# Kernel tuning notes

Hardware: AMD Instinct MI355X
Metric: run time of the kernel (lower is better)

The kernel has to match this reference:

```python
import jax, jax.numpy as jnp
import numpy as np

B = 4096          # number of sessions
MEAN_LEN = 50     # mean items per session
N = B * MEAN_LEN  # total items (ragged lengths sum to this)
H = 256           # feat_input_dim == context_input_dim == hidden_dim


def setup_inputs() -> dict:
    key = jax.random.key(0)
    k1, k2, k3, k4, k5, k6, k7 = jax.random.split(key, 7)
    # ragged lengths in [20, 80] adjusted so they sum exactly to N
    rng = np.random.default_rng(0)
    lens = rng.integers(20, 81, size=B)
    lens = (lens * (N / lens.sum())).astype(np.int64)
    lens[-1] += N - lens.sum()
    s = 1.0 / np.sqrt(H)
    return {
        "feats": jax.random.normal(k1, (N, H), jnp.float32),
        "feat_context": jax.random.normal(k2, (N, H), jnp.float32),
        "batch_num_items": jnp.asarray(lens, jnp.int64),
        "Wu": jax.random.uniform(k3, (H, H), jnp.float32, -s, s),
        "bu": jax.random.uniform(k4, (H,), jnp.float32, -s, s),
        "Wv": jax.random.uniform(k5, (H, H), jnp.float32, -s, s),
        "We": jax.random.uniform(k6, (H,), jnp.float32, -s, s),
        "Wout": jax.random.uniform(k7, (H, H), jnp.float32, -s, s),
    }


def reference(feats, feat_context, batch_num_items, Wu, bu, Wv, We, Wout):
    n = feats.shape[0]
    b = batch_num_items.shape[0]
    # additive attention score per item
    feat_u = feats @ Wu.T + bu                     # [N, H]
    feat_v = feat_context @ Wv.T                   # [N, H]
    e = jax.nn.sigmoid(feat_u + feat_v) @ We       # [N]
    # segment ids from ragged lengths (static total length => jit-safe)
    seg = jnp.repeat(jnp.arange(b), batch_num_items, total_repeat_length=n)
    # segment softmax (numerically stable)
    m = jax.ops.segment_max(e, seg, num_segments=b)        # [B]
    ex = jnp.exp(e - m[seg])                               # [N]
    denom = jax.ops.segment_sum(ex, seg, num_segments=b)   # [B]
    alpha = ex / denom[seg]                                # [N]
    # weighted segment-sum pooling
    rst = jax.ops.segment_sum(feats * alpha[:, None], seg, num_segments=b)  # [B, H]
    return rst @ Wout.T
```

## Files before the change

### kernel.cpp

```cpp
#include <hip/hip_runtime.h>
#include <hip/hip_bf16.h>
#include <cstdint>
#include <cstddef>

#define H 256
#define CHUNK 128

typedef __attribute__((ext_vector_type(8))) short    frag8;
typedef __attribute__((ext_vector_type(4))) float    f32x4;
typedef __attribute__((ext_vector_type(4))) uint32_t u32x4;
typedef __attribute__((ext_vector_type(8))) unsigned short ushort8;

__device__ __forceinline__ unsigned short f32_to_bf16(float f) {
    uint32_t u = __float_as_uint(f);
    u = (u + 0x7FFFu + ((u >> 16) & 1u)) >> 16;
    return (unsigned short)u;
}

__device__ __forceinline__ uint32_t pk_bf16(float a, float b) {
    union { __hip_bfloat162 h2; uint32_t u; } cv;
    cv.h2 = __float22bfloat162_rn(make_float2(a, b));
    return cv.u;
}

__global__ void prep(const float* __restrict__ Wu, const float* __restrict__ Wv,
                     const float* __restrict__ Wout,
                     unsigned short* __restrict__ Wopt, float* __restrict__ WoutT) {
    int bid = blockIdx.x, tid = threadIdx.x;
    if (bid < 64) {
        int idx  = bid * 256 + tid;
        int lane = idx & 63;
        int ct   = (idx >> 6) & 15;
        int ksg  = idx >> 10;
        int col  = ct * 16 + (lane & 15);
        int kg   = ksg * 32 + (lane >> 4) * 8;
        ushort8 pk;
        #pragma unroll
        for (int j = 0; j < 8; j++) {
            int k = kg + j;
            float v = (k < 256) ? Wu[col * 256 + k] : Wv[col * 256 + (k - 256)];
            pk[j] = f32_to_bf16(v);
        }
        *(ushort8*)&Wopt[(size_t)idx * 8] = pk;
    } else {
        int t2 = (bid - 64) * 256 + tid;
        int j = t2 & 255, k = t2 >> 8;
        WoutT[t2] = Wout[j * 256 + k];
    }
}

__global__ void seg_offsets(const int* __restrict__ lens, int B, int* __restrict__ off,
                            int2* __restrict__ chunks, int* __restrict__ chunk_cnt) {
    __shared__ int partL[256], partC[256];
    int tid = threadIdx.x;
    bool is64 = (B >= 3) && (lens[1] == 0) && (lens[3] == 0) && (lens[5] == 0);
    int per = (B + 255) / 256;
    int base = tid * per;
    int sL = 0, sC = 0;
    for (int i = 0; i < per; i++) {
        int idx = base + i;
        if (idx < B) {
            int l = is64 ? lens[2 * idx] : lens[idx];
            sL += l;
            sC += (l + CHUNK - 1) / CHUNK;
        }
    }
    partL[tid] = sL; partC[tid] = sC;
    __syncthreads();
    for (int d = 1; d < 256; d <<= 1) {
        int vL = partL[tid], vC = partC[tid];
        int aL = (tid >= d) ? partL[tid - d] : 0;
        int aC = (tid >= d) ? partC[tid - d] : 0;
        __syncthreads();
        partL[tid] = vL + aL; partC[tid] = vC + aC;
        __syncthreads();
    }
    int runL = partL[tid] - sL;
    int runC = partC[tid] - sC;
    for (int i = 0; i < per; i++) {
        int idx = base + i;
        if (idx < B) {
            int l = is64 ? lens[2 * idx] : lens[idx];
            off[idx] = runL;
            int n = (l + CHUNK - 1) / CHUNK;
            for (int c = 0; c < n; c++)
                chunks[runC + c] = make_int2(idx, runL + c * CHUNK);
            runC += n;
            runL += l;
        }
    }
    if (tid == 255) { off[B] = partL[255]; chunk_cnt[0] = partC[255]; }
}

__global__ __launch_bounds__(512, 4) void fused_e(
        const float* __restrict__ feats, const float* __restrict__ ctx,
        const unsigned short* __restrict__ Wopt,
        const float* __restrict__ bu, const float* __restrict__ We,
        float* __restrict__ e_out, int nTiles) {
    __shared__ unsigned short a_lds[2][64 * 128];
    __shared__ float e_part[8 * 64];

    const int tid  = threadIdx.x;
    const int lane = tid & 63;
    const int w    = tid >> 6;
    const int l15  = lane & 15;
    const int q    = lane >> 4;
    const int r0   = tid >> 3;
    const int c8   = tid & 7;
    const int swz  = r0 & 15;
    const int G    = gridDim.x;

    if (blockIdx.x >= nTiles) return;

    float buv[2], wev[2];
    #pragma unroll
    for (int ci = 0; ci < 2; ++ci) {
        int col = w * 32 + ci * 16 + l15;
        buv[ci] = bu[col];
        wev[ci] = We[col];
    }

    f32x4 acc[4][2];
    #pragma unroll
    for (int i = 0; i < 4; i++)
        #pragma unroll
        for (int j = 0; j < 2; j++)
            acc[i][j] = (f32x4)(0.0f);

    f32x4 pre[4];
    auto loadA = [&](int tile, int kt) {
        const float* s = (kt < 2) ? feats : ctx;
        const float* p = s + ((size_t)tile * 64 + r0) * H + ((kt & 1) << 7) + (c8 << 4);
        pre[0] = *(const f32x4*)p;       pre[1] = *(const f32x4*)(p + 4);
        pre[2] = *(const f32x4*)(p + 8); pre[3] = *(const f32x4*)(p + 12);
    };
    auto cvt_store = [&](int buf) {
        u32x4 g0, g1;
        g0[0] = pk_bf16(pre[0][0], pre[0][1]); g0[1] = pk_bf16(pre[0][2], pre[0][3]);
        g0[2] = pk_bf16(pre[1][0], pre[1][1]); g0[3] = pk_bf16(pre[1][2], pre[1][3]);
        g1[0] = pk_bf16(pre[2][0], pre[2][1]); g1[1] = pk_bf16(pre[2][2], pre[2][3]);
        g1[2] = pk_bf16(pre[3][0], pre[3][1]); g1[3] = pk_bf16(pre[3][2], pre[3][3]);
        *(u32x4*)&a_lds[buf][r0 * 128 + (((2 * c8    ) ^ swz) * 8)] = g0;
        *(u32x4*)&a_lds[buf][r0 * 128 + (((2 * c8 + 1) ^ swz) * 8)] = g1;
    };

    loadA(blockIdx.x, 0);
    cvt_store(0);
    loadA(blockIdx.x, 1);
    __syncthreads();

    int cur = 0;
    for (int tile = blockIdx.x; tile < nTiles; tile += G) {
        #pragma unroll
        for (int kt = 0; kt < 4; ++kt) {
            frag8 bfr[4][2];
            #pragma unroll
            for (int ks = 0; ks < 4; ++ks)
                #pragma unroll
                for (int ci = 0; ci < 2; ++ci)
                    bfr[ks][ci] = *(const frag8*)&Wopt[
                        (((size_t)(kt * 4 + ks) * 16 + (w * 2 + ci)) * 64 + lane) * 8];

            #pragma unroll
            for (int ks = 0; ks < 4; ++ks) {
                frag8 afr[4];
                #pragma unroll
                for (int rt = 0; rt < 4; ++rt)
                    afr[rt] = *(const frag8*)&a_lds[cur][(rt * 16 + l15) * 128 + (((ks * 4 + q) ^ l15) * 8)];
                #pragma unroll
                for (int rt = 0; rt < 4; ++rt)
                    #pragma unroll
                    for (int ci = 0; ci < 2; ++ci)
                        acc[rt][ci] = __builtin_amdgcn_mfma_f32_16x16x32_bf16(
                            afr[rt], bfr[ks][ci], acc[rt][ci], 0, 0, 0);
            }

            const bool last_step = (kt == 3) && (tile + G >= nTiles);
            if (!last_step) {
                cvt_store(cur ^ 1);
                int kt2 = kt + 2, tile2 = tile;
                if (kt2 >= 4) { kt2 -= 4; tile2 += G; }
                if (tile2 < nTiles) loadA(tile2, kt2);
            }
            cur ^= 1;
            __syncthreads();
        }

        #pragma unroll
        for (int rt = 0; rt < 4; ++rt) {
            #pragma unroll
            for (int r = 0; r < 4; ++r) {
                float s = 0.0f;
                #pragma unroll
                for (int ci = 0; ci < 2; ++ci) {
                    float h = acc[rt][ci][r] + buv[ci];
                    s += wev[ci] * __builtin_amdgcn_rcpf(1.0f + __expf(-h));
                    acc[rt][ci][r] = 0.0f;
                }
                s += __shfl_xor(s, 1, 64);
                s += __shfl_xor(s, 2, 64);
                s += __shfl_xor(s, 4, 64);
                s += __shfl_xor(s, 8, 64);
                if (l15 == 0) e_part[w * 64 + rt * 16 + q * 4 + r] = s;
            }
        }
        __syncthreads();
        if (tid < 64) {
            float s = 0.0f;
            #pragma unroll
            for (int ww = 0; ww < 8; ++ww) s += e_part[ww * 64 + tid];
            e_out[(size_t)tile * 64 + tid] = s;
        }
        __syncthreads();
    }
}

__global__ __launch_bounds__(256) void seg_stats(
        float* __restrict__ e, const int* __restrict__ off, int B) {
    int seg = blockIdx.x * 4 + (threadIdx.x >> 6);
    int lane = threadIdx.x & 63;
    if (seg >= B) return;
    int start = off[seg];
    int len = off[seg + 1] - start;
    if (len <= CHUNK) return;
    float m = -3.0e38f;
    for (int i = lane; i < len; i += 64) m = fmaxf(m, e[start + i]);
    #pragma unroll
    for (int o = 32; o > 0; o >>= 1) m = fmaxf(m, __shfl_xor(m, o, 64));
    float s = 0.0f;
    for (int i = lane; i < len; i += 64) s += __expf(e[start + i] - m);
    #pragma unroll
    for (int o = 32; o > 0; o >>= 1) s += __shfl_xor(s, o, 64);
    float inv = (s > 0.0f) ? 1.0f / s : 0.0f;
    for (int i = lane; i < len; i += 64) e[start + i] = __expf(e[start + i] - m) * inv;
}

__global__ __launch_bounds__(256) void pool_chunks(
        const float* __restrict__ ealpha, const float* __restrict__ feats,
        const int* __restrict__ off, const int2* __restrict__ chunks,
        const int* __restrict__ chunk_cnt, float* __restrict__ rst) {
    __shared__ float redf[4 * 256];
    __shared__ float smred[8];
    int idx = blockIdx.x;
    if (idx >= chunk_cnt[0]) return;
    int2 en = chunks[idx];
    int seg = en.x, cstart = en.y;
    int sstart = off[seg], send = off[seg + 1];
    int clen = send - cstart;
    if (clen > CHUNK) clen = CHUNK;
    int tid = threadIdx.x, lane = tid & 63, g = tid >> 6;
    const bool multi = (send - sstart) > CHUNK;

    float m = 0.0f, inv = 1.0f;
    if (!multi) {
        float v = (tid < clen) ? ealpha[cstart + tid] : -3.0e38f;
        #pragma unroll
        for (int o = 32; o > 0; o >>= 1) v = fmaxf(v, __shfl_xor(v, o, 64));
        if (lane == 0) smred[g] = v;
        __syncthreads();
        m = fmaxf(fmaxf(smred[0], smred[1]), fmaxf(smred[2], smred[3]));
        float x = (tid < clen) ? __expf(ealpha[cstart + tid] - m) : 0.0f;
        #pragma unroll
        for (int o = 32; o > 0; o >>= 1) x += __shfl_xor(x, o, 64);
        if (lane == 0) smred[4 + g] = x;
        __syncthreads();
        float ssum = smred[4] + smred[5] + smred[6] + smred[7];
        inv = (ssum > 0.0f) ? 1.0f / ssum : 0.0f;
    }

    const f32x4* F = (const f32x4*)feats + (size_t)cstart * 64 + lane;
    const float* A = ealpha + cstart;
    f32x4 acc0 = (f32x4)(0.0f), acc1 = (f32x4)(0.0f);
    int i = g;
    for (; i + 4 < clen; i += 8) {
        float w0 = A[i], w1 = A[i + 4];
        if (!multi) { w0 = __expf(w0 - m) * inv; w1 = __expf(w1 - m) * inv; }
        acc0 += w0 * F[(size_t)i * 64];
        acc1 += w1 * F[(size_t)(i + 4) * 64];
    }
    if (i < clen) {
        float w0 = A[i];
        if (!multi) w0 = __expf(w0 - m) * inv;
        acc0 += w0 * F[(size_t)i * 64];
    }
    acc0 += acc1;
    *(f32x4*)&redf[g * 256 + lane * 4] = acc0;
    __syncthreads();
    float v = redf[tid] + redf[256 + tid] + redf[512 + tid] + redf[768 + tid];
    if (multi) atomicAdd(&rst[(size_t)seg * H + tid], v);
    else rst[(size_t)seg * H + tid] = v;
}

#define RB 8
__global__ __launch_bounds__(256) void out_gemm(
        const float* __restrict__ rst, const float* __restrict__ WoutT,
        float* __restrict__ out) {
    __shared__ float r[RB * 256];
    const int tid = threadIdx.x;
    const size_t b0 = (size_t)blockIdx.x * RB;
    for (int i = tid; i < RB * 256; i += 256) r[i] = rst[b0 * 256 + i];
    __syncthreads();
    float acc[RB];
    #pragma unroll
    for (int j = 0; j < RB; j++) acc[j] = 0.0f;
    for (int k = 0; k < 256; k += 4) {
        f32x4 rw[RB];
        #pragma unroll
        for (int j = 0; j < RB; j++) rw[j] = *(const f32x4*)&r[j * 256 + k];
        #pragma unroll
        for (int kk = 0; kk < 4; kk++) {
            float wv = WoutT[(size_t)(k + kk) * 256 + tid];
            #pragma unroll
            for (int j = 0; j < RB; j++) acc[j] += rw[j][kk] * wv;
        }
    }
    #pragma unroll
    for (int j = 0; j < RB; j++) out[(b0 + j) * 256 + tid] = acc[j];
}

extern "C" void kernel_launch(void* const* d_in, const int* in_sizes, int n_in,
                              void* d_out, int out_size, void* d_ws, size_t ws_size,
                              hipStream_t stream) {
    const float* feats = (const float*)d_in[0];
    const float* ctx   = (const float*)d_in[1];
    const int*   lens  = (const int*)d_in[2];
    const float* Wu    = (const float*)d_in[3];
    const float* bu    = (const float*)d_in[4];
    const float* Wv    = (const float*)d_in[5];
    const float* We    = (const float*)d_in[6];
    const float* Wout  = (const float*)d_in[7];
    float* out = (float*)d_out;

    const int N = in_sizes[0] / H;
    const int B = in_sizes[2];
    const int maxChunks = B + (N + CHUNK - 1) / CHUNK;
    const int nTiles = N / 64;

    char* w = (char*)d_ws;
    auto carve = [&](size_t bytes) {
        char* p = w;
        w += (bytes + 255) & ~(size_t)255;
        return p;
    };
    int*            off    = (int*)           carve((size_t)(B + 1) * sizeof(int));
    float*          e      = (float*)         carve((size_t)N * sizeof(float));
    float*          rst    = (float*)         carve((size_t)B * H * sizeof(float));
    unsigned short* Wopt   = (unsigned short*)carve((size_t)16 * 16 * 64 * 8 * sizeof(unsigned short));
    float*          WoutT  = (float*)         carve((size_t)H * H * sizeof(float));
    int2*           chunks = (int2*)          carve((size_t)maxChunks * sizeof(int2));
    int*            ccnt   = (int*)           carve(sizeof(int));

    hipMemsetAsync(rst, 0, (size_t)B * H * sizeof(float), stream);

    const int gE = (nTiles < 512) ? nTiles : 512;

    prep        <<<320,         256, 0, stream>>>(Wu, Wv, Wout, Wopt, WoutT);
    seg_offsets <<<1,           256, 0, stream>>>(lens, B, off, chunks, ccnt);
    fused_e     <<<gE,          512, 0, stream>>>(feats, ctx, Wopt, bu, We, e, nTiles);
    seg_stats   <<<(B + 3) / 4, 256, 0, stream>>>(e, off, B);
    pool_chunks <<<maxChunks,   256, 0, stream>>>(e, feats, off, chunks, ccnt, rst);
    out_gemm    <<<B / RB,      256, 0, stream>>>(rst, WoutT, out);
}
```

Measured before the change: 583.7 us.

## Merge prep and scan kernels; launch one block per tile in fused_e

The single-block segment-offset scan is folded into the weight-prep kernel as one extra block, which removes a kernel launch and lets the scan run alongside the weight repacking. fused_e drops its persistent grid-stride loop over tiles and launches one block per 64-row tile (N/64 blocks). Inside each block the four K steps are unrolled, with two register prefetch sets keeping loads ahead of the LDS stores. This removes cross-tile loop overhead and raises parallelism, at the cost of more block launches, reloading the B fragments in every block, and no reuse across tiles.

```diff
diff --git a/kernel.cpp b/kernel.cpp
--- a/kernel.cpp
+++ b/kernel.cpp
@@ -23,9 +23,12 @@
     return cv.u;
 }
 
-__global__ void prep(const float* __restrict__ Wu, const float* __restrict__ Wv,
-                     const float* __restrict__ Wout,
-                     unsigned short* __restrict__ Wopt, float* __restrict__ WoutT) {
+__global__ void prep_scan(const float* __restrict__ Wu, const float* __restrict__ Wv,
+                          const float* __restrict__ Wout,
+                          unsigned short* __restrict__ Wopt, float* __restrict__ WoutT,
+                          const int* __restrict__ lens, int B, int* __restrict__ off,
+                          int2* __restrict__ chunks, int* __restrict__ chunk_cnt) {
+    __shared__ int partL[256], partC[256];
     int bid = blockIdx.x, tid = threadIdx.x;
     if (bid < 64) {
         int idx  = bid * 256 + tid;
@@ -42,61 +45,56 @@
             pk[j] = f32_to_bf16(v);
         }
         *(ushort8*)&Wopt[(size_t)idx * 8] = pk;
-    } else {
+    } else if (bid < 320) {
         int t2 = (bid - 64) * 256 + tid;
         int j = t2 & 255, k = t2 >> 8;
         WoutT[t2] = Wout[j * 256 + k];
-    }
-}
-
-__global__ void seg_offsets(const int* __restrict__ lens, int B, int* __restrict__ off,
-                            int2* __restrict__ chunks, int* __restrict__ chunk_cnt) {
-    __shared__ int partL[256], partC[256];
-    int tid = threadIdx.x;
-    bool is64 = (B >= 3) && (lens[1] == 0) && (lens[3] == 0) && (lens[5] == 0);
-    int per = (B + 255) / 256;
-    int base = tid * per;
-    int sL = 0, sC = 0;
-    for (int i = 0; i < per; i++) {
-        int idx = base + i;
-        if (idx < B) {
-            int l = is64 ? lens[2 * idx] : lens[idx];
-            sL += l;
-            sC += (l + CHUNK - 1) / CHUNK;
-        }
-    }
-    partL[tid] = sL; partC[tid] = sC;
-    __syncthreads();
-    for (int d = 1; d < 256; d <<= 1) {
-        int vL = partL[tid], vC = partC[tid];
-        int aL = (tid >= d) ? partL[tid - d] : 0;
-        int aC = (tid >= d) ? partC[tid - d] : 0;
+    } else {
+        bool is64 = (B >= 3) && (lens[1] == 0) && (lens[3] == 0) && (lens[5] == 0);
+        int per = (B + 255) / 256;
+        int base = tid * per;
+        int sL = 0, sC = 0;
+        for (int i = 0; i < per; i++) {
+            int idx = base + i;
+            if (idx < B) {
+                int l = is64 ? lens[2 * idx] : lens[idx];
+                sL += l;
+                sC += (l + CHUNK - 1) / CHUNK;
+            }
+        }
+        partL[tid] = sL; partC[tid] = sC;
         __syncthreads();
-        partL[tid] = vL + aL; partC[tid] = vC + aC;
-        __syncthreads();
-    }
-    int runL = partL[tid] - sL;
-    int runC = partC[tid] - sC;
-    for (int i = 0; i < per; i++) {
-        int idx = base + i;
-        if (idx < B) {
-            int l = is64 ? lens[2 * idx] : lens[idx];
-            off[idx] = runL;
-            int n = (l + CHUNK - 1) / CHUNK;
-            for (int c = 0; c < n; c++)
-                chunks[runC + c] = make_int2(idx, runL + c * CHUNK);
-            runC += n;
-            runL += l;
-        }
-    }
-    if (tid == 255) { off[B] = partL[255]; chunk_cnt[0] = partC[255]; }
+        for (int d = 1; d < 256; d <<= 1) {
+            int vL = partL[tid], vC = partC[tid];
+            int aL = (tid >= d) ? partL[tid - d] : 0;
+            int aC = (tid >= d) ? partC[tid - d] : 0;
+            __syncthreads();
+            partL[tid] = vL + aL; partC[tid] = vC + aC;
+            __syncthreads();
+        }
+        int runL = partL[tid] - sL;
+        int runC = partC[tid] - sC;
+        for (int i = 0; i < per; i++) {
+            int idx = base + i;
+            if (idx < B) {
+                int l = is64 ? lens[2 * idx] : lens[idx];
+                off[idx] = runL;
+                int n = (l + CHUNK - 1) / CHUNK;
+                for (int c = 0; c < n; c++)
+                    chunks[runC + c] = make_int2(idx, runL + c * CHUNK);
+                runC += n;
+                runL += l;
+            }
+        }
+        if (tid == 255) { off[B] = partL[255]; chunk_cnt[0] = partC[255]; }
+    }
 }
 
 __global__ __launch_bounds__(512, 4) void fused_e(
         const float* __restrict__ feats, const float* __restrict__ ctx,
         const unsigned short* __restrict__ Wopt,
         const float* __restrict__ bu, const float* __restrict__ We,
-        float* __restrict__ e_out, int nTiles) {
+        float* __restrict__ e_out) {
     __shared__ unsigned short a_lds[2][64 * 128];
     __shared__ float e_part[8 * 64];
 
@@ -105,12 +103,10 @@
     const int w    = tid >> 6;
     const int l15  = lane & 15;
     const int q    = lane >> 4;
+    const size_t m0 = (size_t)blockIdx.x * 64;
     const int r0   = tid >> 3;
     const int c8   = tid & 7;
     const int swz  = r0 & 15;
-    const int G    = gridDim.x;
-
-    if (blockIdx.x >= nTiles) return;
 
     float buv[2], wev[2];
     #pragma unroll
@@ -127,92 +123,90 @@
         for (int j = 0; j < 2; j++)
             acc[i][j] = (f32x4)(0.0f);
 
-    f32x4 pre[4];
-    auto loadA = [&](int tile, int kt) {
-        const float* s = (kt < 2) ? feats : ctx;
-        const float* p = s + ((size_t)tile * 64 + r0) * H + ((kt & 1) << 7) + (c8 << 4);
-        pre[0] = *(const f32x4*)p;       pre[1] = *(const f32x4*)(p + 4);
-        pre[2] = *(const f32x4*)(p + 8); pre[3] = *(const f32x4*)(p + 12);
-    };
-    auto cvt_store = [&](int buf) {
-        u32x4 g0, g1;
-        g0[0] = pk_bf16(pre[0][0], pre[0][1]); g0[1] = pk_bf16(pre[0][2], pre[0][3]);
-        g0[2] = pk_bf16(pre[1][0], pre[1][1]); g0[3] = pk_bf16(pre[1][2], pre[1][3]);
-        g1[0] = pk_bf16(pre[2][0], pre[2][1]); g1[1] = pk_bf16(pre[2][2], pre[2][3]);
-        g1[2] = pk_bf16(pre[3][0], pre[3][1]); g1[3] = pk_bf16(pre[3][2], pre[3][3]);
-        *(u32x4*)&a_lds[buf][r0 * 128 + (((2 * c8    ) ^ swz) * 8)] = g0;
-        *(u32x4*)&a_lds[buf][r0 * 128 + (((2 * c8 + 1) ^ swz) * 8)] = g1;
-    };
-
-    loadA(blockIdx.x, 0);
-    cvt_store(0);
-    loadA(blockIdx.x, 1);
-    __syncthreads();
-
-    int cur = 0;
-    for (int tile = blockIdx.x; tile < nTiles; tile += G) {
-        #pragma unroll
-        for (int kt = 0; kt < 4; ++kt) {
-            frag8 bfr[4][2];
-            #pragma unroll
-            for (int ks = 0; ks < 4; ++ks)
-                #pragma unroll
-                for (int ci = 0; ci < 2; ++ci)
-                    bfr[ks][ci] = *(const frag8*)&Wopt[
-                        (((size_t)(kt * 4 + ks) * 16 + (w * 2 + ci)) * 64 + lane) * 8];
-
-            #pragma unroll
-            for (int ks = 0; ks < 4; ++ks) {
-                frag8 afr[4];
-                #pragma unroll
-                for (int rt = 0; rt < 4; ++rt)
-                    afr[rt] = *(const frag8*)&a_lds[cur][(rt * 16 + l15) * 128 + (((ks * 4 + q) ^ l15) * 8)];
-                #pragma unroll
-                for (int rt = 0; rt < 4; ++rt)
-                    #pragma unroll
-                    for (int ci = 0; ci < 2; ++ci)
-                        acc[rt][ci] = __builtin_amdgcn_mfma_f32_16x16x32_bf16(
-                            afr[rt], bfr[ks][ci], acc[rt][ci], 0, 0, 0);
-            }
-
-            const bool last_step = (kt == 3) && (tile + G >= nTiles);
-            if (!last_step) {
-                cvt_store(cur ^ 1);
-                int kt2 = kt + 2, tile2 = tile;
-                if (kt2 >= 4) { kt2 -= 4; tile2 += G; }
-                if (tile2 < nTiles) loadA(tile2, kt2);
-            }
-            cur ^= 1;
-            __syncthreads();
-        }
-
-        #pragma unroll
-        for (int rt = 0; rt < 4; ++rt) {
-            #pragma unroll
-            for (int r = 0; r < 4; ++r) {
-                float s = 0.0f;
-                #pragma unroll
-                for (int ci = 0; ci < 2; ++ci) {
-                    float h = acc[rt][ci][r] + buv[ci];
-                    s += wev[ci] * __builtin_amdgcn_rcpf(1.0f + __expf(-h));
-                    acc[rt][ci][r] = 0.0f;
-                }
-                s += __shfl_xor(s, 1, 64);
-                s += __shfl_xor(s, 2, 64);
-                s += __shfl_xor(s, 4, 64);
-                s += __shfl_xor(s, 8, 64);
-                if (l15 == 0) e_part[w * 64 + rt * 16 + q * 4 + r] = s;
-            }
-        }
-        __syncthreads();
-        if (tid < 64) {
+    f32x4 pa0, pa1, pa2, pa3, pb0, pb1, pb2, pb3;
+
+#define LOADA(d0, d1, d2, d3, kt_) do {                                          \
+    const float* _s = ((kt_) < 2) ? feats : ctx;                                 \
+    const float* _p = _s + (m0 + r0) * H + (((kt_) & 1) << 7) + (c8 << 4);       \
+    d0 = *(const f32x4*)_p;       d1 = *(const f32x4*)(_p + 4);                  \
+    d2 = *(const f32x4*)(_p + 8); d3 = *(const f32x4*)(_p + 12); } while (0)
+
+#define CVTST(buf_, s0, s1, s2, s3) do {                                         \
+    u32x4 g0, g1;                                                                \
+    g0[0] = pk_bf16(s0[0], s0[1]); g0[1] = pk_bf16(s0[2], s0[3]);                \
+    g0[2] = pk_bf16(s1[0], s1[1]); g0[3] = pk_bf16(s1[2], s1[3]);                \
+    g1[0] = pk_bf16(s2[0], s2[1]); g1[1] = pk_bf16(s2[2], s2[3]);                \
+    g1[2] = pk_bf16(s3[0], s3[1]); g1[3] = pk_bf16(s3[2], s3[3]);                \
+    *(u32x4*)&a_lds[buf_][r0 * 128 + (((2 * c8    ) ^ swz) * 8)] = g0;           \
+    *(u32x4*)&a_lds[buf_][r0 * 128 + (((2 * c8 + 1) ^ swz) * 8)] = g1; } while (0)
+
+#define STEP(kt_, buf_) do {                                                     \
+    _Pragma("unroll")                                                            \
+    for (int ks = 0; ks < 4; ++ks) {                                             \
+        frag8 bfr[2];                                                            \
+        _Pragma("unroll")                                                        \
+        for (int ci = 0; ci < 2; ++ci)                                           \
+            bfr[ci] = *(const frag8*)&Wopt[                                      \
+                (((size_t)((kt_) * 4 + ks) * 16 + (w * 2 + ci)) * 64 + lane) * 8]; \
+        frag8 afr[4];                                                            \
+        _Pragma("unroll")                                                        \
+        for (int rt = 0; rt < 4; ++rt)                                           \
+            afr[rt] = *(const frag8*)&a_lds[buf_][(rt * 16 + l15) * 128 +        \
+                                                  (((ks * 4 + q) ^ l15) * 8)];   \
+        _Pragma("unroll")                                                        \
+        for (int rt = 0; rt < 4; ++rt)                                           \
+            _Pragma("unroll")                                                    \
+            for (int ci = 0; ci < 2; ++ci)                                       \
+                acc[rt][ci] = __builtin_amdgcn_mfma_f32_16x16x32_bf16(           \
+                    afr[rt], bfr[ci], acc[rt][ci], 0, 0, 0);                     \
+    } } while (0)
+
+    LOADA(pa0, pa1, pa2, pa3, 0);
+    LOADA(pb0, pb1, pb2, pb3, 1);
+    CVTST(0, pa0, pa1, pa2, pa3);
+    LOADA(pa0, pa1, pa2, pa3, 2);
+    __syncthreads();
+
+    STEP(0, 0);
+    CVTST(1, pb0, pb1, pb2, pb3);
+    LOADA(pb0, pb1, pb2, pb3, 3);
+    __syncthreads();
+
+    STEP(1, 1);
+    CVTST(0, pa0, pa1, pa2, pa3);
+    __syncthreads();
+
+    STEP(2, 0);
+    CVTST(1, pb0, pb1, pb2, pb3);
+    __syncthreads();
+
+    STEP(3, 1);
+
+#undef LOADA
+#undef CVTST
+#undef STEP
+
+    #pragma unroll
+    for (int rt = 0; rt < 4; ++rt) {
+        #pragma unroll
+        for (int r = 0; r < 4; ++r) {
             float s = 0.0f;
             #pragma unroll
-            for (int ww = 0; ww < 8; ++ww) s += e_part[ww * 64 + tid];
-            e_out[(size_t)tile * 64 + tid] = s;
-        }
-        __syncthreads();
-    }
+            for (int ci = 0; ci < 2; ++ci) {
+                float h = acc[rt][ci][r] + buv[ci];
+                s += wev[ci] * __builtin_amdgcn_rcpf(1.0f + __expf(-h));
+            }
+            s += __shfl_xor(s, 1, 64);
+            s += __shfl_xor(s, 2, 64);
+            s += __shfl_xor(s, 4, 64);
+            s += __shfl_xor(s, 8, 64);
+            if (l15 == 0) e_part[w * 64 + rt * 16 + q * 4 + r] = s;
+        }
+    }
+    __syncthreads();
+    if (tid < 64)
+        e_out[m0 + tid] = e_part[tid] + e_part[64 + tid] + e_part[128 + tid] + e_part[192 + tid]
+                        + e_part[256 + tid] + e_part[320 + tid] + e_part[384 + tid] + e_part[448 + tid];
 }
 
 __global__ __launch_bounds__(256) void seg_stats(
@@ -334,7 +328,6 @@
     const int N = in_sizes[0] / H;
     const int B = in_sizes[2];
     const int maxChunks = B + (N + CHUNK - 1) / CHUNK;
-    const int nTiles = N / 64;
 
     char* w = (char*)d_ws;
     auto carve = [&](size_t bytes) {
@@ -352,11 +345,9 @@
 
     hipMemsetAsync(rst, 0, (size_t)B * H * sizeof(float), stream);
 
-    const int gE = (nTiles < 512) ? nTiles : 512;
-
-    prep        <<<320,         256, 0, stream>>>(Wu, Wv, Wout, Wopt, WoutT);
-    seg_offsets <<<1,           256, 0, stream>>>(lens, B, off, chunks, ccnt);
-    fused_e     <<<gE,          512, 0, stream>>>(feats, ctx, Wopt, bu, We, e, nTiles);
+    prep_scan   <<<321,         256, 0, stream>>>(Wu, Wv, Wout, Wopt, WoutT,
+                                                  lens, B, off, chunks, ccnt);
+    fused_e     <<<N / 64,      512, 0, stream>>>(feats, ctx, Wopt, bu, We, e);
     seg_stats   <<<(B + 3) / 4, 256, 0, stream>>>(e, off, B);
     pool_chunks <<<maxChunks,   256, 0, stream>>>(e, feats, off, chunks, ccnt, rst);
     out_gemm    <<<B / RB,      256, 0, stream>>>(rst, WoutT, out);
```

New measurement: 547.1 us. -6.3%, faster.
